# Kernel tuning notes

Hardware: AMD Instinct MI355X
Metric: run time of the kernel (lower is better)

Reference implementation:

```python
import jax, jax.numpy as jnp
import numpy as np
from jax import lax

EPS = 1e-5

@jax.custom_vjp
def binarize(x):
    return jnp.sign(x)

def _bin_fwd(x):
    return jnp.sign(x), x

def _bin_bwd(x, g):
    # straight-through estimator: pass grad where |x| <= 1
    return (g * (jnp.abs(x) <= 1.0).astype(g.dtype),)

binarize.defvjp(_bin_fwd, _bin_bwd)


def bconv(x, w, stride=1, pad=0):
    # BinarizeConv2d: sign-binarize both activations and weights, dense conv
    return lax.conv_general_dilated(
        binarize(x), binarize(w),
        window_strides=(stride, stride),
        padding=[(pad, pad), (pad, pad)],
        dimension_numbers=('NCHW', 'OIHW', 'NCHW'))


def bn(x, gamma, beta):
    # training-mode batch norm (grad enabled in torch forward): batch stats over (N,H,W)
    mean = x.mean(axis=(0, 2, 3), keepdims=True)
    var = ((x - mean) ** 2).mean(axis=(0, 2, 3), keepdims=True)
    return gamma * (x - mean) * lax.rsqrt(var + EPS) + beta


def hardtanh(x):
    return jnp.clip(x, -1.0, 1.0)


def setup_inputs() -> dict:
    key = jax.random.key(0)
    ks = jax.random.split(key, 4)
    N, Cin, H, W = 64, 256, 56, 56
    P = 64  # planes; expansion*planes == Cin -> identity shortcut
    return {
        'x':  jax.random.normal(ks[0], (N, Cin, H, W), dtype=jnp.float32),
        'w1': jax.random.normal(ks[1], (P, Cin, 1, 1), dtype=jnp.float32),
        'w2': jax.random.normal(ks[2], (P, P, 3, 3), dtype=jnp.float32),
        'w3': jax.random.normal(ks[3], (Cin, P, 1, 1), dtype=jnp.float32),
        'g1': jnp.ones((1, P, 1, 1), jnp.float32),
        'b1': jnp.zeros((1, P, 1, 1), jnp.float32),
        'g2': jnp.ones((1, P, 1, 1), jnp.float32),
        'b2': jnp.zeros((1, P, 1, 1), jnp.float32),
        'g3': jnp.ones((1, Cin, 1, 1), jnp.float32),
        'b3': jnp.zeros((1, Cin, 1, 1), jnp.float32),
    }


def reference(x, w1, w2, w3, g1, b1, g2, b2, g3, b3):
    out = hardtanh(bn(bconv(x, w1), g1, b1))                 # 1x1 binconv + BN + hardtanh
    out = hardtanh(bn(bconv(out, w2, stride=1, pad=1), g2, b2))  # 3x3 binconv + BN + hardtanh
    out = bn(bconv(out, w3), g3, b3)                          # 1x1 binconv + BN
    out = out + x                                             # identity shortcut
    return hardtanh(out)
```

## Files before the change

kernel.cpp:

```cpp
#include <hip/hip_runtime.h>
#include <stdint.h>
#include <math.h>

typedef unsigned long long u64;
typedef long long ll;

#define H_    56
#define W_    56
#define HW_   3136
#define N_    64
#define C_    256
#define P_    64
#define NPIX_ 200704
#define BN_EPS 1e-5

__global__ __launch_bounds__(256) void pack_weights_k(
    const float* __restrict__ w1, const float* __restrict__ w2,
    const float* __restrict__ w3,
    u64* __restrict__ ws1, u64* __restrict__ wn1,
    u64* __restrict__ ws2, u64* __restrict__ wn2, int* __restrict__ b2,
    u64* __restrict__ ws3, u64* __restrict__ wn3, int* __restrict__ b3) {
  int t = blockIdx.x * 256 + threadIdx.x;
  if (t < 64) {
    int co = t;
    for (int ch = 0; ch < 4; ++ch) {
      u64 s = 0, n = 0;
      for (int j = 0; j < 64; ++j) {
        float v = w1[co * 256 + ch * 64 + j];
        s |= ((u64)(v < 0.f)) << j;
        n |= ((u64)(v != 0.f)) << j;
      }
      ws1[co * 4 + ch] = s; wn1[co * 4 + ch] = n;
    }
  } else if (t < 64 + 576) {
    int idx = t - 64, co = idx / 9, tap = idx % 9;
    u64 s = 0, n = 0;
    for (int ci = 0; ci < 64; ++ci) {
      float v = w2[(co * 64 + ci) * 9 + tap];
      s |= ((u64)(v < 0.f)) << ci;
      n |= ((u64)(v != 0.f)) << ci;
    }
    ws2[idx] = s; wn2[idx] = n; b2[idx] = __popcll(n);
  } else if (t < 64 + 576 + 256) {
    int co = t - 640;
    u64 s = 0, n = 0;
    for (int ci = 0; ci < 64; ++ci) {
      float v = w3[co * 64 + ci];
      s |= ((u64)(v < 0.f)) << ci;
      n |= ((u64)(v != 0.f)) << ci;
    }
    ws3[co] = s; wn3[co] = n; b3[co] = __popcll(n);
  }
}

__device__ inline void bn_thresh(u64 S_, u64 Q_, float g, float b,
                                 int* A, int* X) {
  double S = (double)(ll)S_, Q = (double)(ll)Q_;
  double mean = S / (double)NPIX_;
  double var  = Q / (double)NPIX_ - mean * mean;
  double sc   = (double)g / sqrt(var + BN_EPS);
  double sh   = (double)b - mean * sc;
  if (sc > 0.0) {
    double t = -sh / sc;
    t = fmin(fmax(t, -1.0e8), 1.0e8);
    *A = (int)ceil(t); *X = 0;
  } else if (sc < 0.0) {
    double t = -sh / sc;
    t = fmin(fmax(t, -1.0e8), 1.0e8);
    *A = (int)floor(t) + 1; *X = 1;
  } else {
    *A = (int)0x80000000; *X = (sh < 0.0) ? 1 : 0;
  }
}

__global__ __launch_bounds__(256) void pack_x_k(
    const float* __restrict__ x, u64* __restrict__ xs, u64* __restrict__ xn) {
  int t = (blockIdx.x >> 2) * 256 + threadIdx.x;
  int q = blockIdx.x & 3;
  int n = t / 1568;
  int pw = (t - n * 1568) * 2;
  const float* xb = x + (size_t)n * (C_ * HW_) + (size_t)(q * 64) * HW_ + pw;
  u64 s0 = 0, s1 = 0, n0 = 0, n1 = 0;
  #pragma unroll 16
  for (int j = 0; j < 64; ++j) {
    float2 v = *(const float2*)(xb + (size_t)j * HW_);
    u64 bit = 1ull << j;
    if (v.x <  0.f) s0 |= bit;
    if (v.x != 0.f) n0 |= bit;
    if (v.y <  0.f) s1 |= bit;
    if (v.y != 0.f) n1 |= bit;
  }
  size_t p = (size_t)t * 2;
  ulonglong2 sv; sv.x = s0; sv.y = s1;
  ulonglong2 nv; nv.x = n0; nv.y = n1;
  *(ulonglong2*)(xs + (size_t)q * NPIX_ + p) = sv;
  *(ulonglong2*)(xn + (size_t)q * NPIX_ + p) = nv;
}

template<int MODE>
__global__ __launch_bounds__(256) void conv1_k(
    const u64* __restrict__ xs, const u64* __restrict__ xn,
    const u64* __restrict__ ws1, const u64* __restrict__ wn1,
    u64* __restrict__ gsum, u64* __restrict__ gsq,
    const float* __restrict__ gamma, const float* __restrict__ beta,
    u64* __restrict__ pout) {
  __shared__ ulonglong2 tile[4][128];
  __shared__ int ssum[64], ssq[64];
  int tid = threadIdx.x, co = tid & 63, wv = tid >> 6;
  int base = blockIdx.x * 128;
  #pragma unroll
  for (int e = tid; e < 512; e += 256) {
    int q = e >> 7, px = e & 127;
    ulonglong2 v;
    v.x = xs[(size_t)q * NPIX_ + base + px];
    v.y = xn[(size_t)q * NPIX_ + base + px];
    tile[q][px] = v;
  }
  if (MODE == 0 && tid < 64) { ssum[tid] = 0; ssq[tid] = 0; }
  u64 wS[4], wN[4];
  #pragma unroll
  for (int q = 0; q < 4; ++q) { wS[q] = ws1[co * 4 + q]; wN[q] = wn1[co * 4 + q]; }
  int A = 0, X = 0;
  if (MODE == 1) bn_thresh(gsum[co], gsq[co], gamma[co], beta[co], &A, &X);
  __syncthreads();
  int s = 0, qq = 0;
  u64 mw = 0;
  #pragma unroll 2
  for (int i = 0; i < 32; ++i) {
    int px = wv * 32 + i;
    int acc = 0;
    #pragma unroll
    for (int q = 0; q < 4; ++q) {
      ulonglong2 t2 = tile[q][px];
      u64 v = t2.y & wN[q];
      u64 a = ~(t2.x ^ wS[q]) & v;
      acc += 2 * __popcll(a) - __popcll(v);
    }
    if (MODE == 0) { s += acc; qq += acc * acc; }
    else {
      u64 bal = __ballot((acc < A) ^ X);
      mw = (co == i) ? bal : mw;
    }
  }
  if (MODE == 0) {
    atomicAdd(&ssum[co], s); atomicAdd(&ssq[co], qq);
    __syncthreads();
    if (tid < 64) {
      atomicAdd(&gsum[tid], (u64)(ll)ssum[tid]);
      atomicAdd(&gsq[tid],  (u64)(ll)ssq[tid]);
    }
  } else {
    if (co < 32) pout[base + wv * 32 + co] = mw;
  }
}

__device__ inline int c2tap(u64 t, u64 ws, u64 wn) {
  return __popcll(~(t ^ ws) & wn);
}

template<int MODE>
__global__ __launch_bounds__(256) void conv2_k(
    const u64* __restrict__ p1,
    const u64* __restrict__ ws2, const u64* __restrict__ wn2,
    u64* __restrict__ gsum, u64* __restrict__ gsq,
    const float* __restrict__ gamma, const float* __restrict__ beta,
    u64* __restrict__ pout) {
  __shared__ u64 tile[6 * W_];
  __shared__ int ssum[64], ssq[64];
  int tid = threadIdx.x, co = tid & 63, wv = tid >> 6;
  int blk = blockIdx.x;
  int n = blk / 14, t0 = blk - n * 14;
  int h0 = t0 * 4;
  const u64* img = p1 + (size_t)n * HW_;
  for (int j = tid; j < 6 * W_; j += 256) {
    int gh = h0 - 1 + j / W_;
    int gw = j - (j / W_) * W_;
    tile[j] = (gh >= 0 && gh < H_) ? img[gh * W_ + gw] : 0ull;
  }
  if (MODE == 0 && tid < 64) { ssum[tid] = 0; ssq[tid] = 0; }
  u64 wS[9], wN[9]; int wB[9], Bs = 0;
  #pragma unroll
  for (int k = 0; k < 9; ++k) {
    wS[k] = ws2[co * 9 + k]; wN[k] = wn2[co * 9 + k];
    wB[k] = __popcll(wN[k]); Bs += wB[k];
  }
  int A = 0, X = 0;
  if (MODE == 1) bn_thresh(gsum[co], gsq[co], gamma[co], beta[co], &A, &X);
  __syncthreads();
  int h = h0 + wv;
  const u64* rA = tile + wv * W_;
  const u64* rB = rA + W_;
  const u64* rC = rB + W_;
  int vA = (h > 0), vC = (h < H_ - 1);
  int s = 0, qq = 0;
  u64 mw = 0;
  if (vA & vC) {
    {
      int P = c2tap(rA[0], wS[1], wN[1]) + c2tap(rA[1], wS[2], wN[2])
            + c2tap(rB[0], wS[4], wN[4]) + c2tap(rB[1], wS[5], wN[5])
            + c2tap(rC[0], wS[7], wN[7]) + c2tap(rC[1], wS[8], wN[8]);
      int acc = 2 * P - (wB[1] + wB[2] + wB[4] + wB[5] + wB[7] + wB[8]);
      if (MODE == 0) { s += acc; qq += acc * acc; }
      else { u64 bal = __ballot((acc < A) ^ X); mw = (co == 0) ? bal : mw; }
    }
    #pragma unroll 2
    for (int w = 1; w < W_ - 1; ++w) {
      int P = c2tap(rA[w-1], wS[0], wN[0]) + c2tap(rA[w], wS[1], wN[1]) + c2tap(rA[w+1], wS[2], wN[2])
            + c2tap(rB[w-1], wS[3], wN[3]) + c2tap(rB[w], wS[4], wN[4]) + c2tap(rB[w+1], wS[5], wN[5])
            + c2tap(rC[w-1], wS[6], wN[6]) + c2tap(rC[w], wS[7], wN[7]) + c2tap(rC[w+1], wS[8], wN[8]);
      int acc = 2 * P - Bs;
      if (MODE == 0) { s += acc; qq += acc * acc; }
      else { u64 bal = __ballot((acc < A) ^ X); mw = (co == w) ? bal : mw; }
    }
    {
      int P = c2tap(rA[W_-2], wS[0], wN[0]) + c2tap(rA[W_-1], wS[1], wN[1])
            + c2tap(rB[W_-2], wS[3], wN[3]) + c2tap(rB[W_-1], wS[4], wN[4])
            + c2tap(rC[W_-2], wS[6], wN[6]) + c2tap(rC[W_-1], wS[7], wN[7]);
      int acc = 2 * P - (wB[0] + wB[1] + wB[3] + wB[4] + wB[6] + wB[7]);
      if (MODE == 0) { s += acc; qq += acc * acc; }
      else { u64 bal = __ballot((acc < A) ^ X); mw = (co == W_ - 1) ? bal : mw; }
    }
  } else {
    for (int w = 0; w < W_; ++w) {
      int wm = w > 0, wp = w < W_ - 1;
      int P = 0, B = 0;
      if (vA) {
        if (wm) { P += c2tap(rA[w-1], wS[0], wN[0]); B += wB[0]; }
        P += c2tap(rA[w], wS[1], wN[1]); B += wB[1];
        if (wp) { P += c2tap(rA[w+1], wS[2], wN[2]); B += wB[2]; }
      }
      if (wm) { P += c2tap(rB[w-1], wS[3], wN[3]); B += wB[3]; }
      P += c2tap(rB[w], wS[4], wN[4]); B += wB[4];
      if (wp) { P += c2tap(rB[w+1], wS[5], wN[5]); B += wB[5]; }
      if (vC) {
        if (wm) { P += c2tap(rC[w-1], wS[6], wN[6]); B += wB[6]; }
        P += c2tap(rC[w], wS[7], wN[7]); B += wB[7];
        if (wp) { P += c2tap(rC[w+1], wS[8], wN[8]); B += wB[8]; }
      }
      int acc = 2 * P - B;
      if (MODE == 0) { s += acc; qq += acc * acc; }
      else { u64 bal = __ballot((acc < A) ^ X); mw = (co == w) ? bal : mw; }
    }
  }
  if (MODE == 0) {
    atomicAdd(&ssum[co], s); atomicAdd(&ssq[co], qq);
    __syncthreads();
    if (tid < 64) {
      atomicAdd(&gsum[tid], (u64)(ll)ssum[tid]);
      atomicAdd(&gsq[tid],  (u64)(ll)ssq[tid]);
    }
  } else {
    if (co < W_) pout[(size_t)n * HW_ + h * W_ + co] = mw;
  }
}

__global__ __launch_bounds__(256) void conv3_stats_k(
    const u64* __restrict__ p2,
    const u64* __restrict__ ws3, const u64* __restrict__ wn3,
    const int* __restrict__ b3,
    u64* __restrict__ gsum, u64* __restrict__ gsq) {
  __shared__ u64 tile[512];
  int t = threadIdx.x;
  int base = blockIdx.x * 512;
  *(ulonglong2*)&tile[t * 2] = *(const ulonglong2*)&p2[base + t * 2];
  u64 s3 = ws3[t], n3 = wn3[t];
  int bb = b3[t];
  __syncthreads();
  int s = 0, q = 0;
  #pragma unroll 4
  for (int i = 0; i < 512; ++i) {
    int yv = 2 * __popcll(~(tile[i] ^ s3) & n3) - bb;
    s += yv; q += yv * yv;
  }
  atomicAdd(&gsum[t], (u64)(ll)s);
  atomicAdd(&gsq[t],  (u64)(ll)q);
}

__global__ __launch_bounds__(256) void thresh3_k(
    const u64* __restrict__ gsum, const u64* __restrict__ gsq,
    const float* __restrict__ gamma, const float* __restrict__ beta,
    float2* __restrict__ tab) {
  int c = threadIdx.x;
  double S = (double)(ll)gsum[c], Q = (double)(ll)gsq[c];
  double mean = S / (double)NPIX_;
  double var  = Q / (double)NPIX_ - mean * mean;
  double inv  = 1.0 / sqrt(var + BN_EPS);
  double sc   = (double)gamma[c] * inv;
  float2 r;
  r.x = (float)sc;
  r.y = (float)((double)beta[c] - mean * sc);
  tab[c] = r;
}

__global__ __launch_bounds__(256) void final_k(
    const float* __restrict__ x, const u64* __restrict__ p2,
    const u64* __restrict__ ws3, const u64* __restrict__ wn3,
    const int* __restrict__ b3, const float2* __restrict__ tab,
    float* __restrict__ out) {
  size_t idx = ((size_t)blockIdx.x * 256 + threadIdx.x) * 4;
  size_t lin = idx / HW_;
  int co = (int)(lin % C_);
  int nn = (int)(lin / C_);
  int hw = (int)(idx % HW_);
  int pb = nn * HW_ + hw;
  u64 s3 = ws3[co], n3 = wn3[co];
  int bb = b3[co];
  float2 th = tab[co];
  float sc = th.x, sh = th.y;
  float4 xv = *(const float4*)(x + idx);
  float4 ov;
  int y0 = 2 * __popcll(~(p2[pb + 0] ^ s3) & n3) - bb;
  int y1 = 2 * __popcll(~(p2[pb + 1] ^ s3) & n3) - bb;
  int y2 = 2 * __popcll(~(p2[pb + 2] ^ s3) & n3) - bb;
  int y3 = 2 * __popcll(~(p2[pb + 3] ^ s3) & n3) - bb;
  ov.x = fminf(fmaxf(sc * (float)y0 + sh + xv.x, -1.f), 1.f);
  ov.y = fminf(fmaxf(sc * (float)y1 + sh + xv.y, -1.f), 1.f);
  ov.z = fminf(fmaxf(sc * (float)y2 + sh + xv.z, -1.f), 1.f);
  ov.w = fminf(fmaxf(sc * (float)y3 + sh + xv.w, -1.f), 1.f);
  *(float4*)(out + idx) = ov;
}

extern "C" void kernel_launch(void* const* d_in, const int* in_sizes, int n_in,
                              void* d_out, int out_size, void* d_ws, size_t ws_size,
                              hipStream_t stream) {
  const float* x  = (const float*)d_in[0];
  const float* w1 = (const float*)d_in[1];
  const float* w2 = (const float*)d_in[2];
  const float* w3 = (const float*)d_in[3];
  const float* g1 = (const float*)d_in[4];
  const float* b1 = (const float*)d_in[5];
  const float* g2 = (const float*)d_in[6];
  const float* b2 = (const float*)d_in[7];
  const float* g3 = (const float*)d_in[8];
  const float* b3 = (const float*)d_in[9];
  float* out = (float*)d_out;

  char* base = (char*)d_ws;
  size_t off = 0;
  auto alloc = [&](size_t bytes) -> char* {
    char* p = base + off;
    off = (off + bytes + 255) & ~(size_t)255;
    return p;
  };
  u64* xs   = (u64*)alloc((size_t)NPIX_ * 4 * 8);
  u64* xnz  = (u64*)alloc((size_t)NPIX_ * 4 * 8);
  u64* p1   = (u64*)alloc((size_t)NPIX_ * 8);
  u64* p2   = (u64*)alloc((size_t)NPIX_ * 8);
  u64* ws1  = (u64*)alloc(256 * 8);
  u64* wn1  = (u64*)alloc(256 * 8);
  u64* ws2  = (u64*)alloc(576 * 8);
  u64* wn2  = (u64*)alloc(576 * 8);
  int* bb2  = (int*)alloc(576 * 4);
  u64* ws3  = (u64*)alloc(256 * 8);
  u64* wn3  = (u64*)alloc(256 * 8);
  int* bb3  = (int*)alloc(256 * 4);
  float2* tab3 = (float2*)alloc(256 * 8);
  char* stats = alloc(768 * 8);
  u64* sum1 = (u64*)stats;          u64* sq1 = sum1 + 64;
  u64* sum2 = sq1 + 64;             u64* sq2 = sum2 + 64;
  u64* sum3 = sq2 + 64;             u64* sq3 = sum3 + 256;
  (void)ws_size; (void)n_in; (void)in_sizes; (void)out_size;

  hipMemsetAsync(stats, 0, 768 * 8, stream);

  pack_weights_k<<<4, 256, 0, stream>>>(w1, w2, w3, ws1, wn1, ws2, wn2, bb2,
                                        ws3, wn3, bb3);

  pack_x_k<<<1568, 256, 0, stream>>>(x, xs, xnz);

  conv1_k<0><<<1568, 256, 0, stream>>>(xs, xnz, ws1, wn1, sum1, sq1,
                                       g1, b1, (u64*)nullptr);
  conv1_k<1><<<1568, 256, 0, stream>>>(xs, xnz, ws1, wn1, sum1, sq1,
                                       g1, b1, p1);

  conv2_k<0><<<896, 256, 0, stream>>>(p1, ws2, wn2, sum2, sq2,
                                      g2, b2, (u64*)nullptr);
  conv2_k<1><<<896, 256, 0, stream>>>(p1, ws2, wn2, sum2, sq2,
                                      g2, b2, p2);

  conv3_stats_k<<<392, 256, 0, stream>>>(p2, ws3, wn3, bb3, sum3, sq3);
  thresh3_k<<<1, 256, 0, stream>>>(sum3, sq3, g3, b3, tab3);

  final_k<<<50176, 256, 0, stream>>>(x, p2, ws3, wn3, bb3, tab3, out);
}
```

Before: 574.9 us.

## Fuse BN threshold computation into stats kernels and conv3 stats into conv2 binarize

```diff
diff --git a/kernel.cpp b/kernel.cpp
--- a/kernel.cpp
+++ b/kernel.cpp
@@ -4,6 +4,7 @@
 
 typedef unsigned long long u64;
 typedef long long ll;
+typedef float f32x4 __attribute__((ext_vector_type(4)));
 
 #define H_    56
 #define W_    56
@@ -97,15 +98,15 @@
   *(ulonglong2*)(xn + (size_t)q * NPIX_ + p) = nv;
 }
 
-template<int MODE>
-__global__ __launch_bounds__(256) void conv1_k(
+__global__ __launch_bounds__(256) void conv1_stats_k(
     const u64* __restrict__ xs, const u64* __restrict__ xn,
     const u64* __restrict__ ws1, const u64* __restrict__ wn1,
     u64* __restrict__ gsum, u64* __restrict__ gsq,
     const float* __restrict__ gamma, const float* __restrict__ beta,
-    u64* __restrict__ pout) {
+    int2* __restrict__ tab, u64* __restrict__ done) {
   __shared__ ulonglong2 tile[4][128];
   __shared__ int ssum[64], ssq[64];
+  __shared__ int amLast;
   int tid = threadIdx.x, co = tid & 63, wv = tid >> 6;
   int base = blockIdx.x * 128;
   #pragma unroll
@@ -116,14 +117,67 @@
     v.y = xn[(size_t)q * NPIX_ + base + px];
     tile[q][px] = v;
   }
-  if (MODE == 0 && tid < 64) { ssum[tid] = 0; ssq[tid] = 0; }
+  if (tid < 64) { ssum[tid] = 0; ssq[tid] = 0; }
   u64 wS[4], wN[4];
   #pragma unroll
   for (int q = 0; q < 4; ++q) { wS[q] = ws1[co * 4 + q]; wN[q] = wn1[co * 4 + q]; }
-  int A = 0, X = 0;
-  if (MODE == 1) bn_thresh(gsum[co], gsq[co], gamma[co], beta[co], &A, &X);
   __syncthreads();
   int s = 0, qq = 0;
+  #pragma unroll 2
+  for (int i = 0; i < 32; ++i) {
+    int px = wv * 32 + i;
+    int acc = 0;
+    #pragma unroll
+    for (int q = 0; q < 4; ++q) {
+      ulonglong2 t2 = tile[q][px];
+      u64 v = t2.y & wN[q];
+      u64 a = ~(t2.x ^ wS[q]) & v;
+      acc += 2 * __popcll(a) - __popcll(v);
+    }
+    s += acc; qq += acc * acc;
+  }
+  atomicAdd(&ssum[co], s); atomicAdd(&ssq[co], qq);
+  __syncthreads();
+  if (tid < 64) {
+    atomicAdd(&gsum[tid], (u64)(ll)ssum[tid]);
+    atomicAdd(&gsq[tid],  (u64)(ll)ssq[tid]);
+  }
+  __syncthreads();
+  if (tid == 0) {
+    __threadfence();
+    amLast = (atomicAdd(done, 1ull) == (u64)(gridDim.x - 1));
+  }
+  __syncthreads();
+  if (amLast && tid < 64) {
+    u64 S = atomicAdd(&gsum[tid], 0ull);
+    u64 Q = atomicAdd(&gsq[tid], 0ull);
+    int A, X;
+    bn_thresh(S, Q, gamma[tid], beta[tid], &A, &X);
+    tab[tid] = make_int2(A, X);
+  }
+}
+
+__global__ __launch_bounds__(256) void bin1_k(
+    const u64* __restrict__ xs, const u64* __restrict__ xn,
+    const u64* __restrict__ ws1, const u64* __restrict__ wn1,
+    const int2* __restrict__ tab, u64* __restrict__ pout) {
+  __shared__ ulonglong2 tile[4][128];
+  int tid = threadIdx.x, co = tid & 63, wv = tid >> 6;
+  int base = blockIdx.x * 128;
+  #pragma unroll
+  for (int e = tid; e < 512; e += 256) {
+    int q = e >> 7, px = e & 127;
+    ulonglong2 v;
+    v.x = xs[(size_t)q * NPIX_ + base + px];
+    v.y = xn[(size_t)q * NPIX_ + base + px];
+    tile[q][px] = v;
+  }
+  u64 wS[4], wN[4];
+  #pragma unroll
+  for (int q = 0; q < 4; ++q) { wS[q] = ws1[co * 4 + q]; wN[q] = wn1[co * 4 + q]; }
+  int2 th = tab[co];
+  int A = th.x, X = th.y;
+  __syncthreads();
   u64 mw = 0;
   #pragma unroll 2
   for (int i = 0; i < 32; ++i) {
@@ -136,37 +190,25 @@
       u64 a = ~(t2.x ^ wS[q]) & v;
       acc += 2 * __popcll(a) - __popcll(v);
     }
-    if (MODE == 0) { s += acc; qq += acc * acc; }
-    else {
-      u64 bal = __ballot((acc < A) ^ X);
-      mw = (co == i) ? bal : mw;
-    }
-  }
-  if (MODE == 0) {
-    atomicAdd(&ssum[co], s); atomicAdd(&ssq[co], qq);
-    __syncthreads();
-    if (tid < 64) {
-      atomicAdd(&gsum[tid], (u64)(ll)ssum[tid]);
-      atomicAdd(&gsq[tid],  (u64)(ll)ssq[tid]);
-    }
-  } else {
-    if (co < 32) pout[base + wv * 32 + co] = mw;
-  }
+    u64 bal = __ballot((acc < A) ^ X);
+    mw = (co == i) ? bal : mw;
+  }
+  if (co < 32) pout[base + wv * 32 + co] = mw;
 }
 
 __device__ inline int c2tap(u64 t, u64 ws, u64 wn) {
   return __popcll(~(t ^ ws) & wn);
 }
 
-template<int MODE>
-__global__ __launch_bounds__(256) void conv2_k(
+__global__ __launch_bounds__(256) void conv2_stats_k(
     const u64* __restrict__ p1,
     const u64* __restrict__ ws2, const u64* __restrict__ wn2,
     u64* __restrict__ gsum, u64* __restrict__ gsq,
     const float* __restrict__ gamma, const float* __restrict__ beta,
-    u64* __restrict__ pout) {
+    int2* __restrict__ tab, u64* __restrict__ done) {
   __shared__ u64 tile[6 * W_];
   __shared__ int ssum[64], ssq[64];
+  __shared__ int amLast;
   int tid = threadIdx.x, co = tid & 63, wv = tid >> 6;
   int blk = blockIdx.x;
   int n = blk / 14, t0 = blk - n * 14;
@@ -177,15 +219,13 @@
     int gw = j - (j / W_) * W_;
     tile[j] = (gh >= 0 && gh < H_) ? img[gh * W_ + gw] : 0ull;
   }
-  if (MODE == 0 && tid < 64) { ssum[tid] = 0; ssq[tid] = 0; }
+  if (tid < 64) { ssum[tid] = 0; ssq[tid] = 0; }
   u64 wS[9], wN[9]; int wB[9], Bs = 0;
   #pragma unroll
   for (int k = 0; k < 9; ++k) {
     wS[k] = ws2[co * 9 + k]; wN[k] = wn2[co * 9 + k];
     wB[k] = __popcll(wN[k]); Bs += wB[k];
   }
-  int A = 0, X = 0;
-  if (MODE == 1) bn_thresh(gsum[co], gsq[co], gamma[co], beta[co], &A, &X);
   __syncthreads();
   int h = h0 + wv;
   const u64* rA = tile + wv * W_;
@@ -193,103 +233,184 @@
   const u64* rC = rB + W_;
   int vA = (h > 0), vC = (h < H_ - 1);
   int s = 0, qq = 0;
+  if (vA & vC) {
+    {
+      int Pp = c2tap(rA[0], wS[1], wN[1]) + c2tap(rA[1], wS[2], wN[2])
+             + c2tap(rB[0], wS[4], wN[4]) + c2tap(rB[1], wS[5], wN[5])
+             + c2tap(rC[0], wS[7], wN[7]) + c2tap(rC[1], wS[8], wN[8]);
+      int acc = 2 * Pp - (wB[1] + wB[2] + wB[4] + wB[5] + wB[7] + wB[8]);
+      s += acc; qq += acc * acc;
+    }
+    #pragma unroll 2
+    for (int w = 1; w < W_ - 1; ++w) {
+      int Pp = c2tap(rA[w-1], wS[0], wN[0]) + c2tap(rA[w], wS[1], wN[1]) + c2tap(rA[w+1], wS[2], wN[2])
+             + c2tap(rB[w-1], wS[3], wN[3]) + c2tap(rB[w], wS[4], wN[4]) + c2tap(rB[w+1], wS[5], wN[5])
+             + c2tap(rC[w-1], wS[6], wN[6]) + c2tap(rC[w], wS[7], wN[7]) + c2tap(rC[w+1], wS[8], wN[8]);
+      int acc = 2 * Pp - Bs;
+      s += acc; qq += acc * acc;
+    }
+    {
+      int Pp = c2tap(rA[W_-2], wS[0], wN[0]) + c2tap(rA[W_-1], wS[1], wN[1])
+             + c2tap(rB[W_-2], wS[3], wN[3]) + c2tap(rB[W_-1], wS[4], wN[4])
+             + c2tap(rC[W_-2], wS[6], wN[6]) + c2tap(rC[W_-1], wS[7], wN[7]);
+      int acc = 2 * Pp - (wB[0] + wB[1] + wB[3] + wB[4] + wB[6] + wB[7]);
+      s += acc; qq += acc * acc;
+    }
+  } else {
+    for (int w = 0; w < W_; ++w) {
+      int wm = w > 0, wp = w < W_ - 1;
+      int Pp = 0, B = 0;
+      if (vA) {
+        if (wm) { Pp += c2tap(rA[w-1], wS[0], wN[0]); B += wB[0]; }
+        Pp += c2tap(rA[w], wS[1], wN[1]); B += wB[1];
+        if (wp) { Pp += c2tap(rA[w+1], wS[2], wN[2]); B += wB[2]; }
+      }
+      if (wm) { Pp += c2tap(rB[w-1], wS[3], wN[3]); B += wB[3]; }
+      Pp += c2tap(rB[w], wS[4], wN[4]); B += wB[4];
+      if (wp) { Pp += c2tap(rB[w+1], wS[5], wN[5]); B += wB[5]; }
+      if (vC) {
+        if (wm) { Pp += c2tap(rC[w-1], wS[6], wN[6]); B += wB[6]; }
+        Pp += c2tap(rC[w], wS[7], wN[7]); B += wB[7];
+        if (wp) { Pp += c2tap(rC[w+1], wS[8], wN[8]); B += wB[8]; }
+      }
+      int acc = 2 * Pp - B;
+      s += acc; qq += acc * acc;
+    }
+  }
+  atomicAdd(&ssum[co], s); atomicAdd(&ssq[co], qq);
+  __syncthreads();
+  if (tid < 64) {
+    atomicAdd(&gsum[tid], (u64)(ll)ssum[tid]);
+    atomicAdd(&gsq[tid],  (u64)(ll)ssq[tid]);
+  }
+  __syncthreads();
+  if (tid == 0) {
+    __threadfence();
+    amLast = (atomicAdd(done, 1ull) == (u64)(gridDim.x - 1));
+  }
+  __syncthreads();
+  if (amLast && tid < 64) {
+    u64 S = atomicAdd(&gsum[tid], 0ull);
+    u64 Q = atomicAdd(&gsq[tid], 0ull);
+    int A, X;
+    bn_thresh(S, Q, gamma[tid], beta[tid], &A, &X);
+    tab[tid] = make_int2(A, X);
+  }
+}
+
+__global__ __launch_bounds__(256) void bin2c3_k(
+    const u64* __restrict__ p1,
+    const u64* __restrict__ ws2, const u64* __restrict__ wn2,
+    const int2* __restrict__ tab2, u64* __restrict__ pout,
+    const u64* __restrict__ ws3, const u64* __restrict__ wn3,
+    const int* __restrict__ b3,
+    u64* __restrict__ gsum3, u64* __restrict__ gsq3,
+    const float* __restrict__ g3, const float* __restrict__ b3f,
+    float2* __restrict__ tab3, u64* __restrict__ done) {
+  __shared__ u64 tile[6 * W_];
+  __shared__ u64 outw[4 * W_];
+  __shared__ int amLast;
+  int tid = threadIdx.x, co = tid & 63, wv = tid >> 6;
+  int blk = blockIdx.x;
+  int n = blk / 14, t0 = blk - n * 14;
+  int h0 = t0 * 4;
+  const u64* img = p1 + (size_t)n * HW_;
+  for (int j = tid; j < 6 * W_; j += 256) {
+    int gh = h0 - 1 + j / W_;
+    int gw = j - (j / W_) * W_;
+    tile[j] = (gh >= 0 && gh < H_) ? img[gh * W_ + gw] : 0ull;
+  }
+  u64 wS[9], wN[9]; int wB[9], Bs = 0;
+  #pragma unroll
+  for (int k = 0; k < 9; ++k) {
+    wS[k] = ws2[co * 9 + k]; wN[k] = wn2[co * 9 + k];
+    wB[k] = __popcll(wN[k]); Bs += wB[k];
+  }
+  int2 th = tab2[co];
+  int A = th.x, X = th.y;
+  __syncthreads();
+  int h = h0 + wv;
+  const u64* rA = tile + wv * W_;
+  const u64* rB = rA + W_;
+  const u64* rC = rB + W_;
+  int vA = (h > 0), vC = (h < H_ - 1);
   u64 mw = 0;
   if (vA & vC) {
     {
-      int P = c2tap(rA[0], wS[1], wN[1]) + c2tap(rA[1], wS[2], wN[2])
-            + c2tap(rB[0], wS[4], wN[4]) + c2tap(rB[1], wS[5], wN[5])
-            + c2tap(rC[0], wS[7], wN[7]) + c2tap(rC[1], wS[8], wN[8]);
-      int acc = 2 * P - (wB[1] + wB[2] + wB[4] + wB[5] + wB[7] + wB[8]);
-      if (MODE == 0) { s += acc; qq += acc * acc; }
-      else { u64 bal = __ballot((acc < A) ^ X); mw = (co == 0) ? bal : mw; }
+      int Pp = c2tap(rA[0], wS[1], wN[1]) + c2tap(rA[1], wS[2], wN[2])
+             + c2tap(rB[0], wS[4], wN[4]) + c2tap(rB[1], wS[5], wN[5])
+             + c2tap(rC[0], wS[7], wN[7]) + c2tap(rC[1], wS[8], wN[8]);
+      int acc = 2 * Pp - (wB[1] + wB[2] + wB[4] + wB[5] + wB[7] + wB[8]);
+      u64 bal = __ballot((acc < A) ^ X); mw = (co == 0) ? bal : mw;
     }
     #pragma unroll 2
     for (int w = 1; w < W_ - 1; ++w) {
-      int P = c2tap(rA[w-1], wS[0], wN[0]) + c2tap(rA[w], wS[1], wN[1]) + c2tap(rA[w+1], wS[2], wN[2])
-            + c2tap(rB[w-1], wS[3], wN[3]) + c2tap(rB[w], wS[4], wN[4]) + c2tap(rB[w+1], wS[5], wN[5])
-            + c2tap(rC[w-1], wS[6], wN[6]) + c2tap(rC[w], wS[7], wN[7]) + c2tap(rC[w+1], wS[8], wN[8]);
-      int acc = 2 * P - Bs;
-      if (MODE == 0) { s += acc; qq += acc * acc; }
-      else { u64 bal = __ballot((acc < A) ^ X); mw = (co == w) ? bal : mw; }
+      int Pp = c2tap(rA[w-1], wS[0], wN[0]) + c2tap(rA[w], wS[1], wN[1]) + c2tap(rA[w+1], wS[2], wN[2])
+             + c2tap(rB[w-1], wS[3], wN[3]) + c2tap(rB[w], wS[4], wN[4]) + c2tap(rB[w+1], wS[5], wN[5])
+             + c2tap(rC[w-1], wS[6], wN[6]) + c2tap(rC[w], wS[7], wN[7]) + c2tap(rC[w+1], wS[8], wN[8]);
+      int acc = 2 * Pp - Bs;
+      u64 bal = __ballot((acc < A) ^ X); mw = (co == w) ? bal : mw;
     }
     {
-      int P = c2tap(rA[W_-2], wS[0], wN[0]) + c2tap(rA[W_-1], wS[1], wN[1])
-            + c2tap(rB[W_-2], wS[3], wN[3]) + c2tap(rB[W_-1], wS[4], wN[4])
-            + c2tap(rC[W_-2], wS[6], wN[6]) + c2tap(rC[W_-1], wS[7], wN[7]);
-      int acc = 2 * P - (wB[0] + wB[1] + wB[3] + wB[4] + wB[6] + wB[7]);
-      if (MODE == 0) { s += acc; qq += acc * acc; }
-      else { u64 bal = __ballot((acc < A) ^ X); mw = (co == W_ - 1) ? bal : mw; }
+      int Pp = c2tap(rA[W_-2], wS[0], wN[0]) + c2tap(rA[W_-1], wS[1], wN[1])
+             + c2tap(rB[W_-2], wS[3], wN[3]) + c2tap(rB[W_-1], wS[4], wN[4])
+             + c2tap(rC[W_-2], wS[6], wN[6]) + c2tap(rC[W_-1], wS[7], wN[7]);
+      int acc = 2 * Pp - (wB[0] + wB[1] + wB[3] + wB[4] + wB[6] + wB[7]);
+      u64 bal = __ballot((acc < A) ^ X); mw = (co == W_ - 1) ? bal : mw;
     }
   } else {
     for (int w = 0; w < W_; ++w) {
       int wm = w > 0, wp = w < W_ - 1;
-      int P = 0, B = 0;
+      int Pp = 0, B = 0;
       if (vA) {
-        if (wm) { P += c2tap(rA[w-1], wS[0], wN[0]); B += wB[0]; }
-        P += c2tap(rA[w], wS[1], wN[1]); B += wB[1];
-        if (wp) { P += c2tap(rA[w+1], wS[2], wN[2]); B += wB[2]; }
+        if (wm) { Pp += c2tap(rA[w-1], wS[0], wN[0]); B += wB[0]; }
+        Pp += c2tap(rA[w], wS[1], wN[1]); B += wB[1];
+        if (wp) { Pp += c2tap(rA[w+1], wS[2], wN[2]); B += wB[2]; }
       }
-      if (wm) { P += c2tap(rB[w-1], wS[3], wN[3]); B += wB[3]; }
-      P += c2tap(rB[w], wS[4], wN[4]); B += wB[4];
-      if (wp) { P += c2tap(rB[w+1], wS[5], wN[5]); B += wB[5]; }
+      if (wm) { Pp += c2tap(rB[w-1], wS[3], wN[3]); B += wB[3]; }
+      Pp += c2tap(rB[w], wS[4], wN[4]); B += wB[4];
+      if (wp) { Pp += c2tap(rB[w+1], wS[5], wN[5]); B += wB[5]; }
       if (vC) {
-        if (wm) { P += c2tap(rC[w-1], wS[6], wN[6]); B += wB[6]; }
-        P += c2tap(rC[w], wS[7], wN[7]); B += wB[7];
-        if (wp) { P += c2tap(rC[w+1], wS[8], wN[8]); B += wB[8]; }
+        if (wm) { Pp += c2tap(rC[w-1], wS[6], wN[6]); B += wB[6]; }
+        Pp += c2tap(rC[w], wS[7], wN[7]); B += wB[7];
+        if (wp) { Pp += c2tap(rC[w+1], wS[8], wN[8]); B += wB[8]; }
       }
-      int acc = 2 * P - B;
-      if (MODE == 0) { s += acc; qq += acc * acc; }
-      else { u64 bal = __ballot((acc < A) ^ X); mw = (co == w) ? bal : mw; }
-    }
-  }
-  if (MODE == 0) {
-    atomicAdd(&ssum[co], s); atomicAdd(&ssq[co], qq);
-    __syncthreads();
-    if (tid < 64) {
-      atomicAdd(&gsum[tid], (u64)(ll)ssum[tid]);
-      atomicAdd(&gsq[tid],  (u64)(ll)ssq[tid]);
-    }
-  } else {
-    if (co < W_) pout[(size_t)n * HW_ + h * W_ + co] = mw;
-  }
-}
-
-__global__ __launch_bounds__(256) void conv3_stats_k(
-    const u64* __restrict__ p2,
-    const u64* __restrict__ ws3, const u64* __restrict__ wn3,
-    const int* __restrict__ b3,
-    u64* __restrict__ gsum, u64* __restrict__ gsq) {
-  __shared__ u64 tile[512];
-  int t = threadIdx.x;
-  int base = blockIdx.x * 512;
-  *(ulonglong2*)&tile[t * 2] = *(const ulonglong2*)&p2[base + t * 2];
-  u64 s3 = ws3[t], n3 = wn3[t];
-  int bb = b3[t];
-  __syncthreads();
+      int acc = 2 * Pp - B;
+      u64 bal = __ballot((acc < A) ^ X); mw = (co == w) ? bal : mw;
+    }
+  }
+  if (co < W_) {
+    pout[(size_t)n * HW_ + h * W_ + co] = mw;
+    outw[wv * W_ + co] = mw;
+  }
+  __syncthreads();
+  u64 s3 = ws3[tid], n3 = wn3[tid];
+  int bb = b3[tid];
   int s = 0, q = 0;
   #pragma unroll 4
-  for (int i = 0; i < 512; ++i) {
-    int yv = 2 * __popcll(~(tile[i] ^ s3) & n3) - bb;
+  for (int i = 0; i < 4 * W_; ++i) {
+    int yv = 2 * __popcll(~(outw[i] ^ s3) & n3) - bb;
     s += yv; q += yv * yv;
   }
-  atomicAdd(&gsum[t], (u64)(ll)s);
-  atomicAdd(&gsq[t],  (u64)(ll)q);
-}
-
-__global__ __launch_bounds__(256) void thresh3_k(
-    const u64* __restrict__ gsum, const u64* __restrict__ gsq,
-    const float* __restrict__ gamma, const float* __restrict__ beta,
-    float2* __restrict__ tab) {
-  int c = threadIdx.x;
-  double S = (double)(ll)gsum[c], Q = (double)(ll)gsq[c];
-  double mean = S / (double)NPIX_;
-  double var  = Q / (double)NPIX_ - mean * mean;
-  double inv  = 1.0 / sqrt(var + BN_EPS);
-  double sc   = (double)gamma[c] * inv;
-  float2 r;
-  r.x = (float)sc;
-  r.y = (float)((double)beta[c] - mean * sc);
-  tab[c] = r;
+  atomicAdd(&gsum3[tid], (u64)(ll)s);
+  atomicAdd(&gsq3[tid],  (u64)(ll)q);
+  __syncthreads();
+  if (tid == 0) {
+    __threadfence();
+    amLast = (atomicAdd(done, 1ull) == (u64)(gridDim.x - 1));
+  }
+  __syncthreads();
+  if (amLast) {
+    u64 S = atomicAdd(&gsum3[tid], 0ull);
+    u64 Q = atomicAdd(&gsq3[tid], 0ull);
+    double mean = (double)(ll)S / (double)NPIX_;
+    double var  = (double)(ll)Q / (double)NPIX_ - mean * mean;
+    double sc   = (double)g3[tid] / sqrt(var + BN_EPS);
+    float2 r;
+    r.x = (float)sc;
+    r.y = (float)((double)b3f[tid] - mean * sc);
+    tab3[tid] = r;
+  }
 }
 
 __global__ __launch_bounds__(256) void final_k(
@@ -297,7 +418,7 @@
     const u64* __restrict__ ws3, const u64* __restrict__ wn3,
     const int* __restrict__ b3, const float2* __restrict__ tab,
     float* __restrict__ out) {
-  size_t idx = ((size_t)blockIdx.x * 256 + threadIdx.x) * 4;
+  size_t idx = ((size_t)blockIdx.x * 256 + threadIdx.x) * 8;
   size_t lin = idx / HW_;
   int co = (int)(lin % C_);
   int nn = (int)(lin / C_);
@@ -307,17 +428,23 @@
   int bb = b3[co];
   float2 th = tab[co];
   float sc = th.x, sh = th.y;
-  float4 xv = *(const float4*)(x + idx);
-  float4 ov;
-  int y0 = 2 * __popcll(~(p2[pb + 0] ^ s3) & n3) - bb;
-  int y1 = 2 * __popcll(~(p2[pb + 1] ^ s3) & n3) - bb;
-  int y2 = 2 * __popcll(~(p2[pb + 2] ^ s3) & n3) - bb;
-  int y3 = 2 * __popcll(~(p2[pb + 3] ^ s3) & n3) - bb;
-  ov.x = fminf(fmaxf(sc * (float)y0 + sh + xv.x, -1.f), 1.f);
-  ov.y = fminf(fmaxf(sc * (float)y1 + sh + xv.y, -1.f), 1.f);
-  ov.z = fminf(fmaxf(sc * (float)y2 + sh + xv.z, -1.f), 1.f);
-  ov.w = fminf(fmaxf(sc * (float)y3 + sh + xv.w, -1.f), 1.f);
-  *(float4*)(out + idx) = ov;
+  float4 xa = *(const float4*)(x + idx);
+  float4 xb = *(const float4*)(x + idx + 4);
+  int yv[8];
+  #pragma unroll
+  for (int j = 0; j < 8; ++j)
+    yv[j] = 2 * __popcll(~(p2[pb + j] ^ s3) & n3) - bb;
+  f32x4 oa, ob;
+  oa.x = fminf(fmaxf(sc * (float)yv[0] + sh + xa.x, -1.f), 1.f);
+  oa.y = fminf(fmaxf(sc * (float)yv[1] + sh + xa.y, -1.f), 1.f);
+  oa.z = fminf(fmaxf(sc * (float)yv[2] + sh + xa.z, -1.f), 1.f);
+  oa.w = fminf(fmaxf(sc * (float)yv[3] + sh + xa.w, -1.f), 1.f);
+  ob.x = fminf(fmaxf(sc * (float)yv[4] + sh + xb.x, -1.f), 1.f);
+  ob.y = fminf(fmaxf(sc * (float)yv[5] + sh + xb.y, -1.f), 1.f);
+  ob.z = fminf(fmaxf(sc * (float)yv[6] + sh + xb.z, -1.f), 1.f);
+  ob.w = fminf(fmaxf(sc * (float)yv[7] + sh + xb.w, -1.f), 1.f);
+  __builtin_nontemporal_store(oa, (f32x4*)(out + idx));
+  __builtin_nontemporal_store(ob, (f32x4*)(out + idx + 4));
 }
 
 extern "C" void kernel_launch(void* const* d_in, const int* in_sizes, int n_in,
@@ -354,32 +481,33 @@
   u64* ws3  = (u64*)alloc(256 * 8);
   u64* wn3  = (u64*)alloc(256 * 8);
   int* bb3  = (int*)alloc(256 * 4);
+  int2* tab1 = (int2*)alloc(64 * 8);
+  int2* tab2 = (int2*)alloc(64 * 8);
   float2* tab3 = (float2*)alloc(256 * 8);
-  char* stats = alloc(768 * 8);
+  char* stats = alloc(792 * 8);
   u64* sum1 = (u64*)stats;          u64* sq1 = sum1 + 64;
   u64* sum2 = sq1 + 64;             u64* sq2 = sum2 + 64;
   u64* sum3 = sq2 + 64;             u64* sq3 = sum3 + 256;
+  u64* done1 = sq3 + 256;           u64* done2 = done1 + 1;
+  u64* done3 = done2 + 1;
   (void)ws_size; (void)n_in; (void)in_sizes; (void)out_size;
 
-  hipMemsetAsync(stats, 0, 768 * 8, stream);
+  hipMemsetAsync(stats, 0, 792 * 8, stream);
 
   pack_weights_k<<<4, 256, 0, stream>>>(w1, w2, w3, ws1, wn1, ws2, wn2, bb2,
                                         ws3, wn3, bb3);
 
   pack_x_k<<<1568, 256, 0, stream>>>(x, xs, xnz);
 
-  conv1_k<0><<<1568, 256, 0, stream>>>(xs, xnz, ws1, wn1, sum1, sq1,
-                                       g1, b1, (u64*)nullptr);
-  conv1_k<1><<<1568, 256, 0, stream>>>(xs, xnz, ws1, wn1, sum1, sq1,
-                                       g1, b1, p1);
-
-  conv2_k<0><<<896, 256, 0, stream>>>(p1, ws2, wn2, sum2, sq2,
-                                      g2, b2, (u64*)nullptr);
-  conv2_k<1><<<896, 256, 0, stream>>>(p1, ws2, wn2, sum2, sq2,
-                                      g2, b2, p2);
-
-  conv3_stats_k<<<392, 256, 0, stream>>>(p2, ws3, wn3, bb3, sum3, sq3);
-  thresh3_k<<<1, 256, 0, stream>>>(sum3, sq3, g3, b3, tab3);
-
-  final_k<<<50176, 256, 0, stream>>>(x, p2, ws3, wn3, bb3, tab3, out);
-}
+  conv1_stats_k<<<1568, 256, 0, stream>>>(xs, xnz, ws1, wn1, sum1, sq1,
+                                          g1, b1, tab1, done1);
+  bin1_k<<<1568, 256, 0, stream>>>(xs, xnz, ws1, wn1, tab1, p1);
+
+  conv2_stats_k<<<896, 256, 0, stream>>>(p1, ws2, wn2, sum2, sq2,
+                                         g2, b2, tab2, done2);
+  bin2c3_k<<<896, 256, 0, stream>>>(p1, ws2, wn2, tab2, p2,
+                                    ws3, wn3, bb3, sum3, sq3,
+                                    g3, b3, tab3, done3);
+
+  final_k<<<25088, 256, 0, stream>>>(x, p2, ws3, wn3, bb3, tab3, out);
+}
```

Result: faster. 562.6 us (-2.1%).
